# Kernel optimization log

Measured on AMD Instinct MI355X. Metric: run time of the kernel, lower is better.

The kernel has to match this reference:

```python
import jax, jax.numpy as jnp
import numpy as np

N = 100000
E = 1600000
D = 64
EPS = 1e-5


def setup_inputs() -> dict:
    key = jax.random.key(0)
    ks = jax.random.split(key, 16)
    edge_index = jax.random.randint(ks[0], (2, E), 0, N, dtype=jnp.int64)
    node_attr = jax.random.normal(ks[1], (N, D), dtype=jnp.float32)
    edge_attr = jax.random.normal(ks[2], (E, D), dtype=jnp.float32)
    scale = 1.0 / np.sqrt(D)
    params = {}
    for i, k in enumerate(range(3, 3 + 3)):
        li = i + 1
        kw, kb = jax.random.split(ks[k])
        params[f"W{li}"] = jax.random.uniform(kw, (D, D), jnp.float32, -scale, scale)
        params[f"b{li}"] = jax.random.uniform(kb, (D,), jnp.float32, -scale, scale)
        params[f"gamma{li}"] = jnp.ones((D,), jnp.float32)
        params[f"beta{li}"] = jnp.zeros((D,), jnp.float32)
    return {"edge_index": edge_index, "node_attr": node_attr, "edge_attr": edge_attr, **params}


def _gcn_conv(x, src, dst, dinv, W, b):
    # GCNConv: h = D^{-1/2} (A + I) D^{-1/2} (x W) + b  (symmetric norm, self-loops)
    h = x @ W  # [N, D]
    norm = (dinv[src] * dinv[dst])[:, None]  # [E, 1]
    agg = jax.ops.segment_sum(h[src] * norm, dst, num_segments=N)  # neighbor messages
    agg = agg + (dinv * dinv)[:, None] * h  # self-loop contribution
    return agg + b


def _bn(x, gamma, beta):
    # BatchNorm1d in training mode: batch statistics over the node dimension
    mean = jnp.mean(x, axis=0)
    var = jnp.var(x, axis=0)
    return gamma * (x - mean) * jax.lax.rsqrt(var + EPS) + beta


def reference(edge_index, node_attr, edge_attr,
              W1, b1, gamma1, beta1,
              W2, b2, gamma2, beta2,
              W3, b3, gamma3, beta3):
    src, dst = edge_index[0], edge_index[1]
    # degree including self-loop (PyG gcn_norm: deg computed at target + 1)
    deg = jnp.zeros((N,), jnp.float32).at[dst].add(1.0) + 1.0
    dinv = jax.lax.rsqrt(deg)
    x = _bn(jax.nn.relu(_gcn_conv(node_attr, src, dst, dinv, W1, b1)), gamma1, beta1)
    x = _bn(jax.nn.relu(_gcn_conv(x, src, dst, dinv, W2, b2)), gamma2, beta2)
    x = _bn(jax.nn.relu(_gcn_conv(x, src, dst, dinv, W3, b3)), gamma3, beta3)
    return x
```

## Files before the change

kernel.cpp:

```cpp
#include <hip/hip_runtime.h>

#define N_NODES 100000
#define N_EDGES 1600000
#define D 64
#define EPS 1e-5f


#define SCAN_BLOCKS 128
#define SCAN_T 256

__global__ void detect_kernel(const unsigned* __restrict__ ei, int* __restrict__ flag) {
    int t = threadIdx.x;
    unsigned stride = (2u * (unsigned)N_EDGES) / 256u;
    unsigned w = (unsigned)t * stride + 1u;
    unsigned v = ei[w];
    __shared__ unsigned red[256];
    red[t] = v;
    __syncthreads();
    for (int s = 128; s > 0; s >>= 1) {
        if (t < s) red[t] |= red[t + s];
        __syncthreads();
    }
    if (t == 0) *flag = (red[0] == 0u) ? 1 : 0;
}

__device__ __forceinline__ int load_idx(const void* ei, int is64, size_t pos) {
    if (is64) return (int)((const long long*)ei)[pos];
    return ((const int*)ei)[pos];
}

__global__ void degcount_kernel(const void* __restrict__ ei, const int* __restrict__ flag,
                                float* __restrict__ deg) {
    int e = blockIdx.x * 256 + threadIdx.x;
    if (e >= N_EDGES) return;
    int is64 = *flag;
    int d = load_idx(ei, is64, (size_t)N_EDGES + e);
    atomicAdd(&deg[d], 1.0f);
}

__global__ void dinv_kernel(const float* __restrict__ deg, float* __restrict__ dinv) {
    int n = blockIdx.x * 256 + threadIdx.x;
    if (n >= N_NODES) return;
    dinv[n] = rsqrtf(deg[n] + 1.0f);
}

__global__ void scanA_kernel(const float* __restrict__ deg, int* __restrict__ bsum) {
    int b = blockIdx.x, t = threadIdx.x;
    const int chunk = (N_NODES + SCAN_BLOCKS - 1) / SCAN_BLOCKS;
    const int tchunk = (chunk + SCAN_T - 1) / SCAN_T;
    int lo = b * chunk + t * tchunk;
    int hi = min(lo + tchunk, min((b + 1) * chunk, N_NODES));
    int s = 0;
    for (int i = lo; i < hi; ++i) s += (int)deg[i];
    __shared__ int red[SCAN_T];
    red[t] = s;
    __syncthreads();
    for (int st = 128; st > 0; st >>= 1) {
        if (t < st) red[t] += red[t + st];
        __syncthreads();
    }
    if (t == 0) bsum[b] = red[0];
}

__global__ void scanB_kernel(int* __restrict__ bsum) {
    __shared__ int sh[SCAN_BLOCKS];
    int t = threadIdx.x;
    sh[t] = bsum[t];
    __syncthreads();
    for (int st = 1; st < SCAN_BLOCKS; st <<= 1) {
        int v = (t >= st) ? sh[t - st] : 0;
        __syncthreads();
        sh[t] += v;
        __syncthreads();
    }
    bsum[t] = (t == 0) ? 0 : sh[t - 1];
}

__global__ void scanC_kernel(const float* __restrict__ deg, const int* __restrict__ bsum,
                             int* __restrict__ off, int* __restrict__ cursor) {
    int b = blockIdx.x, t = threadIdx.x;
    const int chunk = (N_NODES + SCAN_BLOCKS - 1) / SCAN_BLOCKS;
    const int tchunk = (chunk + SCAN_T - 1) / SCAN_T;
    int lo = b * chunk + t * tchunk;
    int hi = min(lo + tchunk, min((b + 1) * chunk, N_NODES));
    int s = 0;
    for (int i = lo; i < hi; ++i) s += (int)deg[i];
    __shared__ int red[SCAN_T];
    red[t] = s;
    __syncthreads();
    for (int st = 1; st < SCAN_T; st <<= 1) {
        int v = (t >= st) ? red[t - st] : 0;
        __syncthreads();
        red[t] += v;
        __syncthreads();
    }
    int tbase = bsum[b] + red[t] - s;
    for (int i = lo; i < hi; ++i) {
        int d = (int)deg[i];
        off[i] = tbase;
        cursor[i] = tbase;
        tbase += d;
    }
    if (b == 0 && t == 0) off[N_NODES] = N_EDGES;
}

__global__ void bucket_kernel(const void* __restrict__ ei, const int* __restrict__ flag,
                              const float* __restrict__ dinv, int* __restrict__ cursor,
                              long long* __restrict__ packed) {
    int e = blockIdx.x * 256 + threadIdx.x;
    if (e >= N_EDGES) return;
    int is64 = *flag;
    int s = load_idx(ei, is64, e);
    int d = load_idx(ei, is64, (size_t)N_EDGES + e);
    int pos = atomicAdd(&cursor[d], 1);
    unsigned long long pk =
        (unsigned long long)(unsigned)s |
        ((unsigned long long)__float_as_uint(dinv[s]) << 32);
    packed[pos] = (long long)pk;
}

__global__ __launch_bounds__(256) void gemm_kernel(const float* __restrict__ x,
                                                   const float* __restrict__ W,
                                                   float* __restrict__ h) {
    int lane = threadIdx.x & 63;
    int wv = threadIdx.x >> 6;
    float wcol[64];
#pragma unroll
    for (int k = 0; k < 64; ++k) wcol[k] = W[k * 64 + lane];
    int row0 = blockIdx.x * 64;
    for (int r = wv; r < 64; r += 4) {
        int row = row0 + r;
        if (row >= N_NODES) break;
        const float* xr = x + (size_t)row * 64;
        float acc = 0.f;
#pragma unroll
        for (int k = 0; k < 64; ++k) acc += xr[k] * wcol[k];
        h[(size_t)row * 64 + lane] = acc;
    }
}

__global__ __launch_bounds__(256) void gather_kernel(const float* __restrict__ h,
                                                     const int* __restrict__ off,
                                                     const long long* __restrict__ packed,
                                                     const float* __restrict__ dinv,
                                                     const float* __restrict__ b,
                                                     float* __restrict__ agg) {
    int lane = threadIdx.x & 63;
    int wv = threadIdx.x >> 6;
    int n = blockIdx.x * 4 + wv;
    if (n >= N_NODES) return;
    float dn = dinv[n];
    float acc = dn * dn * h[(size_t)n * 64 + lane] + b[lane];
    int j0 = off[n], j1 = off[n + 1];
    for (int j = j0; j < j1; ++j) {
        long long pk = packed[j];
        int s = (int)(pk & 0xffffffffLL);
        float ds = __int_as_float((int)(pk >> 32));
        acc += (ds * dn) * h[(size_t)s * 64 + lane];
    }
    agg[(size_t)n * 64 + lane] = acc;
}

__global__ __launch_bounds__(256) void stats_kernel(const float* __restrict__ agg,
                                                    float* __restrict__ stats) {
    int lane = threadIdx.x & 63;
    int sub = threadIdx.x >> 6;
    float s1 = 0.f, s2 = 0.f;
    for (int r = blockIdx.x * 4 + sub; r < N_NODES; r += gridDim.x * 4) {
        float v = agg[(size_t)r * 64 + lane];
        v = fmaxf(v, 0.f);
        s1 += v;
        s2 += v * v;
    }
    __shared__ float red[2][4][64];
    red[0][sub][lane] = s1;
    red[1][sub][lane] = s2;
    __syncthreads();
    if (sub == 0) {
        s1 = red[0][0][lane] + red[0][1][lane] + red[0][2][lane] + red[0][3][lane];
        s2 = red[1][0][lane] + red[1][1][lane] + red[1][2][lane] + red[1][3][lane];
        atomicAdd(&stats[lane], s1);
        atomicAdd(&stats[64 + lane], s2);
    }
}

__global__ __launch_bounds__(256) void apply_kernel(const float* __restrict__ agg,
                                                    const float* __restrict__ stats,
                                                    const float* __restrict__ gamma,
                                                    const float* __restrict__ beta,
                                                    float* __restrict__ out) {
    int i = blockIdx.x * 256 + threadIdx.x;
    if (i >= N_NODES * 16) return;
    int d0 = (i & 15) << 2;
    float4 v = reinterpret_cast<const float4*>(agg)[i];
    float r[4] = {v.x, v.y, v.z, v.w};
    float4 o;
    float* op = &o.x;
    const float invN = 1.0f / (float)N_NODES;
#pragma unroll
    for (int j = 0; j < 4; ++j) {
        int d = d0 + j;
        float mean = stats[d] * invN;
        float var = stats[64 + d] * invN - mean * mean;
        float rs = rsqrtf(var + EPS);
        float val = fmaxf(r[j], 0.f);
        op[j] = gamma[d] * (val - mean) * rs + beta[d];
    }
    reinterpret_cast<float4*>(out)[i] = o;
}

extern "C" void kernel_launch(void* const* d_in, const int* in_sizes, int n_in,
                              void* d_out, int out_size, void* d_ws, size_t ws_size,
                              hipStream_t stream) {
    const void* ei = d_in[0];
    const float* node_attr = (const float*)d_in[1];

    char* ws = (char*)d_ws;
    int* flag = (int*)(ws + 0);
    float* deg = (float*)(ws + 256);
    float* dinv = (float*)(ws + 400256);
    int* off = (int*)(ws + 800256);
    int* bsum = (int*)(ws + 1200320);
    int* cursor = (int*)(ws + 1200832);
    float* stats = (float*)(ws + 1600832);
    long long* packed = (long long*)(ws + 1601536);
    float* h = (float*)(ws + 14401536);
    float* agg = (float*)(ws + 40001536);
    float* xbuf = (float*)(ws + 65601536);

    hipMemsetAsync(deg, 0, (size_t)N_NODES * 4, stream);
    detect_kernel<<<1, 256, 0, stream>>>((const unsigned*)ei, flag);
    degcount_kernel<<<N_EDGES / 256, 256, 0, stream>>>(ei, flag, deg);
    dinv_kernel<<<(N_NODES + 255) / 256, 256, 0, stream>>>(deg, dinv);
    scanA_kernel<<<SCAN_BLOCKS, SCAN_T, 0, stream>>>(deg, bsum);
    scanB_kernel<<<1, SCAN_BLOCKS, 0, stream>>>(bsum);
    scanC_kernel<<<SCAN_BLOCKS, SCAN_T, 0, stream>>>(deg, bsum, off, cursor);
    bucket_kernel<<<N_EDGES / 256, 256, 0, stream>>>(ei, flag, dinv, cursor, packed);

    const float* x = node_attr;
    for (int l = 0; l < 3; ++l) {
        const float* W = (const float*)d_in[3 + 4 * l];
        const float* b = (const float*)d_in[4 + 4 * l];
        const float* gamma = (const float*)d_in[5 + 4 * l];
        const float* beta = (const float*)d_in[6 + 4 * l];

        gemm_kernel<<<(N_NODES + 63) / 64, 256, 0, stream>>>(x, W, h);
        gather_kernel<<<(N_NODES + 3) / 4, 256, 0, stream>>>(h, off, packed, dinv, b, agg);
        hipMemsetAsync(stats, 0, 512, stream);
        stats_kernel<<<1024, 256, 0, stream>>>(agg, stats);
        float* outp = (l == 2) ? (float*)d_out : xbuf;
        apply_kernel<<<(N_NODES * 16 + 255) / 256, 256, 0, stream>>>(agg, stats, gamma, beta, outp);
        x = xbuf;
    }
}
```

Baseline: 1.424 ms.

## Vectorize gather with float4 edge-parallel lanes and fuse setup kernels

The gather kernel now splits each wavefront into four groups of 16 lanes. Each group handles a different edge and loads the neighbour row as float4, and the groups' partial sums are combined with xor-shuffles. This raises memory-level parallelism in the main aggregation loop, at the cost of idle lanes when a node's degree is not a multiple of four. Separately, the memsets and the detect kernel merge into one setup kernel, the dinv computation moves into the first scan kernel, degree counting switches to integer atomics, per-layer stats buffers replace the per-layer memset, and bucket writes use nontemporal stores, all to cut launches and small overheads.

```diff
diff --git a/kernel.cpp b/kernel.cpp
--- a/kernel.cpp
+++ b/kernel.cpp
@@ -9,19 +9,24 @@
 #define SCAN_BLOCKS 128
 #define SCAN_T 256
 
-__global__ void detect_kernel(const unsigned* __restrict__ ei, int* __restrict__ flag) {
-    int t = threadIdx.x;
-    unsigned stride = (2u * (unsigned)N_EDGES) / 256u;
-    unsigned w = (unsigned)t * stride + 1u;
-    unsigned v = ei[w];
-    __shared__ unsigned red[256];
-    red[t] = v;
-    __syncthreads();
-    for (int s = 128; s > 0; s >>= 1) {
-        if (t < s) red[t] |= red[t + s];
-        __syncthreads();
-    }
-    if (t == 0) *flag = (red[0] == 0u) ? 1 : 0;
+__global__ void setup_kernel(const unsigned* __restrict__ ei, int* __restrict__ flag,
+                             int* __restrict__ deg, float* __restrict__ stats) {
+    int t = blockIdx.x * 256 + threadIdx.x;
+    if (t < N_NODES) deg[t] = 0;
+    if (t < 384) stats[t] = 0.f;
+    if (blockIdx.x == gridDim.x - 1) {
+        int tt = threadIdx.x;
+        unsigned stride = (2u * (unsigned)N_EDGES) / 256u;
+        unsigned v = ei[(unsigned)tt * stride + 1u];
+        __shared__ unsigned red[256];
+        red[tt] = v;
+        __syncthreads();
+        for (int s = 128; s > 0; s >>= 1) {
+            if (tt < s) red[tt] |= red[tt + s];
+            __syncthreads();
+        }
+        if (tt == 0) *flag = (red[0] == 0u) ? 1 : 0;
+    }
 }
 
 __device__ __forceinline__ int load_idx(const void* ei, int is64, size_t pos) {
@@ -30,28 +35,27 @@
 }
 
 __global__ void degcount_kernel(const void* __restrict__ ei, const int* __restrict__ flag,
-                                float* __restrict__ deg) {
+                                int* __restrict__ deg) {
     int e = blockIdx.x * 256 + threadIdx.x;
     if (e >= N_EDGES) return;
     int is64 = *flag;
     int d = load_idx(ei, is64, (size_t)N_EDGES + e);
-    atomicAdd(&deg[d], 1.0f);
-}
-
-__global__ void dinv_kernel(const float* __restrict__ deg, float* __restrict__ dinv) {
-    int n = blockIdx.x * 256 + threadIdx.x;
-    if (n >= N_NODES) return;
-    dinv[n] = rsqrtf(deg[n] + 1.0f);
-}
-
-__global__ void scanA_kernel(const float* __restrict__ deg, int* __restrict__ bsum) {
+    atomicAdd(&deg[d], 1);
+}
+
+__global__ void scanA_kernel(const int* __restrict__ deg, float* __restrict__ dinv,
+                             int* __restrict__ bsum) {
     int b = blockIdx.x, t = threadIdx.x;
     const int chunk = (N_NODES + SCAN_BLOCKS - 1) / SCAN_BLOCKS;
     const int tchunk = (chunk + SCAN_T - 1) / SCAN_T;
     int lo = b * chunk + t * tchunk;
     int hi = min(lo + tchunk, min((b + 1) * chunk, N_NODES));
     int s = 0;
-    for (int i = lo; i < hi; ++i) s += (int)deg[i];
+    for (int i = lo; i < hi; ++i) {
+        int d = deg[i];
+        s += d;
+        dinv[i] = rsqrtf((float)d + 1.0f);
+    }
     __shared__ int red[SCAN_T];
     red[t] = s;
     __syncthreads();
@@ -76,7 +80,7 @@
     bsum[t] = (t == 0) ? 0 : sh[t - 1];
 }
 
-__global__ void scanC_kernel(const float* __restrict__ deg, const int* __restrict__ bsum,
+__global__ void scanC_kernel(const int* __restrict__ deg, const int* __restrict__ bsum,
                              int* __restrict__ off, int* __restrict__ cursor) {
     int b = blockIdx.x, t = threadIdx.x;
     const int chunk = (N_NODES + SCAN_BLOCKS - 1) / SCAN_BLOCKS;
@@ -84,7 +88,7 @@
     int lo = b * chunk + t * tchunk;
     int hi = min(lo + tchunk, min((b + 1) * chunk, N_NODES));
     int s = 0;
-    for (int i = lo; i < hi; ++i) s += (int)deg[i];
+    for (int i = lo; i < hi; ++i) s += deg[i];
     __shared__ int red[SCAN_T];
     red[t] = s;
     __syncthreads();
@@ -96,7 +100,7 @@
     }
     int tbase = bsum[b] + red[t] - s;
     for (int i = lo; i < hi; ++i) {
-        int d = (int)deg[i];
+        int d = deg[i];
         off[i] = tbase;
         cursor[i] = tbase;
         tbase += d;
@@ -116,7 +120,7 @@
     unsigned long long pk =
         (unsigned long long)(unsigned)s |
         ((unsigned long long)__float_as_uint(dinv[s]) << 32);
-    packed[pos] = (long long)pk;
+    __builtin_nontemporal_store((long long)pk, &packed[pos]);
 }
 
 __global__ __launch_bounds__(256) void gemm_kernel(const float* __restrict__ x,
@@ -149,16 +153,42 @@
     int wv = threadIdx.x >> 6;
     int n = blockIdx.x * 4 + wv;
     if (n >= N_NODES) return;
+    int g = lane >> 4;
+    int fq = lane & 15;
     float dn = dinv[n];
-    float acc = dn * dn * h[(size_t)n * 64 + lane] + b[lane];
+    float4 acc = make_float4(0.f, 0.f, 0.f, 0.f);
     int j0 = off[n], j1 = off[n + 1];
-    for (int j = j0; j < j1; ++j) {
-        long long pk = packed[j];
-        int s = (int)(pk & 0xffffffffLL);
-        float ds = __int_as_float((int)(pk >> 32));
-        acc += (ds * dn) * h[(size_t)s * 64 + lane];
-    }
-    agg[(size_t)n * 64 + lane] = acc;
+    for (int j = j0; j < j1; j += 4) {
+        int jj = j + g;
+        if (jj < j1) {
+            long long pk = packed[jj];
+            int s = (int)(pk & 0xffffffffLL);
+            float w = __int_as_float((int)(pk >> 32)) * dn;
+            float4 hv = reinterpret_cast<const float4*>(h + (size_t)s * 64)[fq];
+            acc.x += w * hv.x;
+            acc.y += w * hv.y;
+            acc.z += w * hv.z;
+            acc.w += w * hv.w;
+        }
+    }
+#pragma unroll
+    for (int m = 16; m <= 32; m <<= 1) {
+        acc.x += __shfl_xor(acc.x, m, 64);
+        acc.y += __shfl_xor(acc.y, m, 64);
+        acc.z += __shfl_xor(acc.z, m, 64);
+        acc.w += __shfl_xor(acc.w, m, 64);
+    }
+    if (g == 0) {
+        float4 hv = reinterpret_cast<const float4*>(h + (size_t)n * 64)[fq];
+        float4 bv = reinterpret_cast<const float4*>(b)[fq];
+        float sw = dn * dn;
+        float4 o;
+        o.x = acc.x + sw * hv.x + bv.x;
+        o.y = acc.y + sw * hv.y + bv.y;
+        o.z = acc.z + sw * hv.z + bv.z;
+        o.w = acc.w + sw * hv.w + bv.w;
+        reinterpret_cast<float4*>(agg + (size_t)n * 64)[fq] = o;
+    }
 }
 
 __global__ __launch_bounds__(256) void stats_kernel(const float* __restrict__ agg,
@@ -217,22 +247,20 @@
 
     char* ws = (char*)d_ws;
     int* flag = (int*)(ws + 0);
-    float* deg = (float*)(ws + 256);
+    int* deg = (int*)(ws + 256);
     float* dinv = (float*)(ws + 400256);
     int* off = (int*)(ws + 800256);
-    int* bsum = (int*)(ws + 1200320);
-    int* cursor = (int*)(ws + 1200832);
-    float* stats = (float*)(ws + 1600832);
-    long long* packed = (long long*)(ws + 1601536);
-    float* h = (float*)(ws + 14401536);
-    float* agg = (float*)(ws + 40001536);
-    float* xbuf = (float*)(ws + 65601536);
-
-    hipMemsetAsync(deg, 0, (size_t)N_NODES * 4, stream);
-    detect_kernel<<<1, 256, 0, stream>>>((const unsigned*)ei, flag);
+    int* bsum = (int*)(ws + 1200384);
+    int* cursor = (int*)(ws + 1200896);
+    float* stats = (float*)(ws + 1600896);
+    long long* packed = (long long*)(ws + 1602432);
+    float* h = (float*)(ws + 14402432);
+    float* agg = (float*)(ws + 40002432);
+    float* xbuf = (float*)(ws + 65602432);
+
+    setup_kernel<<<(N_NODES + 255) / 256, 256, 0, stream>>>((const unsigned*)ei, flag, deg, stats);
     degcount_kernel<<<N_EDGES / 256, 256, 0, stream>>>(ei, flag, deg);
-    dinv_kernel<<<(N_NODES + 255) / 256, 256, 0, stream>>>(deg, dinv);
-    scanA_kernel<<<SCAN_BLOCKS, SCAN_T, 0, stream>>>(deg, bsum);
+    scanA_kernel<<<SCAN_BLOCKS, SCAN_T, 0, stream>>>(deg, dinv, bsum);
     scanB_kernel<<<1, SCAN_BLOCKS, 0, stream>>>(bsum);
     scanC_kernel<<<SCAN_BLOCKS, SCAN_T, 0, stream>>>(deg, bsum, off, cursor);
     bucket_kernel<<<N_EDGES / 256, 256, 0, stream>>>(ei, flag, dinv, cursor, packed);
@@ -243,13 +271,13 @@
         const float* b = (const float*)d_in[4 + 4 * l];
         const float* gamma = (const float*)d_in[5 + 4 * l];
         const float* beta = (const float*)d_in[6 + 4 * l];
+        float* stats_l = stats + 128 * l;
 
         gemm_kernel<<<(N_NODES + 63) / 64, 256, 0, stream>>>(x, W, h);
         gather_kernel<<<(N_NODES + 3) / 4, 256, 0, stream>>>(h, off, packed, dinv, b, agg);
-        hipMemsetAsync(stats, 0, 512, stream);
-        stats_kernel<<<1024, 256, 0, stream>>>(agg, stats);
+        stats_kernel<<<1024, 256, 0, stream>>>(agg, stats_l);
         float* outp = (l == 2) ? (float*)d_out : xbuf;
-        apply_kernel<<<(N_NODES * 16 + 255) / 256, 256, 0, stream>>>(agg, stats, gamma, beta, outp);
+        apply_kernel<<<(N_NODES * 16 + 255) / 256, 256, 0, stream>>>(agg, stats_l, gamma, beta, outp);
         x = xbuf;
     }
 }
```

Result: faster. 1.169 ms (-17.9%).
